# Kernel tuning notes

Hardware: AMD Instinct MI355X
Metric: run time of the kernel (lower is better)

The kernel has to match this reference:

```python
import jax, jax.numpy as jnp
import numpy as np

N = 1048576  # rays * samples per batch
IN_DIM = 32          # hashgrid encoder output (16 levels x 2 feats)
SH_DIM = 16          # degree-4 spherical harmonics
HID = 64
GEO = 15


def sh_encode(v):
    """Real spherical harmonics up to degree 4 (16 comps), v: [N,3] unit vecs."""
    x, y, z = v[..., 0], v[..., 1], v[..., 2]
    xx, yy, zz = x * x, y * y, z * z
    xy, yz, xz = x * y, y * z, x * z
    comps = [
        jnp.full_like(x, 0.28209479177387814),
        -0.48860251190291987 * y,
        0.48860251190291987 * z,
        -0.48860251190291987 * x,
        1.0925484305920792 * xy,
        -1.0925484305920792 * yz,
        0.94617469575755997 * zz - 0.31539156525252005,
        -1.0925484305920792 * xz,
        0.54627421529603959 * (xx - yy),
        0.59004358992664352 * y * (3.0 * xx - yy),
        2.8906114426405538 * xy * z,
        0.45704579946446572 * y * (4.0 * zz - xx - yy),
        0.3731763325901154 * z * (2.0 * zz - 3.0 * xx - 3.0 * yy),
        0.45704579946446572 * x * (4.0 * zz - xx - yy),
        1.445305721320277 * z * (xx - yy),
        0.5900435899266435 * x * (xx - 3.0 * yy),
    ]
    return jnp.stack(comps, axis=-1)


def _w(key, fan_in, fan_out):
    return jax.random.normal(key, (fan_in, fan_out), dtype=jnp.float32) / np.sqrt(fan_in)


def setup_inputs() -> dict:
    key = jax.random.key(0)
    ks = jax.random.split(key, 12)
    x_feat = jax.random.normal(ks[0], (N, IN_DIM), dtype=jnp.float32)
    d = jax.random.normal(ks[1], (N, 3), dtype=jnp.float32)
    d = d / jnp.linalg.norm(d, axis=-1, keepdims=True)
    lig = jax.random.normal(ks[2], (N, 3), dtype=jnp.float32)
    lig = lig / jnp.linalg.norm(lig, axis=-1, keepdims=True)
    return {
        "x_feat": x_feat, "d": d, "lig": lig,
        # sigma net: 32 -> 64 -> 1+15
        "w_sig0": _w(ks[3], IN_DIM, HID),
        "w_sig1": _w(ks[4], HID, 1 + GEO),
        # color net: (16+16+32) -> 64, (64+15) -> 64, 64 -> 3
        "w_col0": _w(ks[5], SH_DIM + SH_DIM + IN_DIM, HID),
        "w_col1": _w(ks[6], HID + GEO, HID),
        "w_col2": _w(ks[7], HID, 3),
        # vis net (only 2 layers run in forward): (16+32) -> 64, 64 -> 1
        "w_vis0": _w(ks[8], SH_DIM + IN_DIM, HID),
        "w_vis1": _w(ks[9], HID, 1),
    }


def reference(x_feat, d, lig, w_sig0, w_sig1, w_col0, w_col1, w_col2, w_vis0, w_vis1):
    # sigma tower (bias-free)
    h = jax.nn.relu(x_feat @ w_sig0)
    h = h @ w_sig1                      # [N, 1+GEO]
    geo_feat = h[..., 1:]               # sigma = trunc_exp(h[...,0]) is unused in output

    d_enc = sh_encode(d)                # [N,16]
    l_enc = sh_encode(lig)              # [N,16]

    # color tower: cat([h_x, light, d]) then cat geo_feat before layer 1
    hc = jnp.concatenate([x_feat, l_enc, d_enc], axis=-1)
    hc = jax.nn.relu(hc @ w_col0)
    hc = jnp.concatenate([hc, geo_feat], axis=-1)
    hc = jax.nn.relu(hc @ w_col1)
    hc = hc @ w_col2
    color = jax.nn.relu(hc)             # [N,3]

    # vis tower: cat([h_x, light]), 2 layers (range(num_layers))
    hv = jnp.concatenate([x_feat, l_enc], axis=-1)
    hv = jax.nn.relu(hv @ w_vis0)
    hv = hv @ w_vis1
    vis = jax.nn.sigmoid(hv)            # [N,1]

    return color * vis                  # broadcast -> [N,3]
```

## Files before the change

kernel.cpp:

```cpp
#include <hip/hip_runtime.h>
#include <math.h>

#define BLOCK 256
#define GRID  512

typedef _Float16 half8 __attribute__((ext_vector_type(8)));
typedef float    f32x4 __attribute__((ext_vector_type(4)));

__device__ __forceinline__ int phi(int nt, int m) {
    return ((nt >> 1) << 5) + ((m >> 2) << 3) + ((nt & 1) << 2) + (m & 3);
}

__device__ __forceinline__ half8 bfragW(const float* __restrict__ w, int N0,
                                        int nsrc, int k0, int Kreal, bool valid) {
    half8 r;
    #pragma unroll
    for (int j = 0; j < 8; j++) {
        int k = k0 + j;
        float v = (valid && k < Kreal) ? w[k * N0 + nsrc] : 0.f;
        r[j] = (_Float16)v;
    }
    return r;
}

__device__ __forceinline__ half8 packrelu(f32x4 a, f32x4 b) {
    half8 h;
    #pragma unroll
    for (int r = 0; r < 4; r++) {
        h[r]     = (_Float16)fmaxf(a[r], 0.f);
        h[4 + r] = (_Float16)fmaxf(b[r], 0.f);
    }
    return h;
}

__device__ __forceinline__ half8 packraw(f32x4 a, f32x4 b) {
    half8 h;
    #pragma unroll
    for (int r = 0; r < 4; r++) {
        h[r]     = (_Float16)a[r];
        h[4 + r] = (_Float16)b[r];
    }
    return h;
}

__device__ __forceinline__ void sh16(float x, float y, float z, float* e) {
    float xx = x * x, yy = y * y, zz = z * z;
    float xy = x * y, yz = y * z, xz = x * z;
    e[0]  = 0.28209479177387814f;
    e[1]  = -0.48860251190291987f * y;
    e[2]  = 0.48860251190291987f * z;
    e[3]  = -0.48860251190291987f * x;
    e[4]  = 1.0925484305920792f * xy;
    e[5]  = -1.0925484305920792f * yz;
    e[6]  = 0.94617469575756f * zz - 0.31539156525252005f;
    e[7]  = -1.0925484305920792f * xz;
    e[8]  = 0.5462742152960396f * (xx - yy);
    e[9]  = 0.5900435899266435f * y * (3.0f * xx - yy);
    e[10] = 2.890611442640554f * xy * z;
    e[11] = 0.4570457994644657f * y * (4.0f * zz - xx - yy);
    e[12] = 0.3731763325901154f * z * (2.0f * zz - 3.0f * xx - 3.0f * yy);
    e[13] = 0.4570457994644657f * x * (4.0f * zz - xx - yy);
    e[14] = 1.445305721320277f * z * (xx - yy);
    e[15] = 0.5900435899266435f * x * (xx - 3.0f * yy);
}

#define MFMA(A, B, C) __builtin_amdgcn_mfma_f32_16x16x32_f16((A), (B), (C), 0, 0, 0)

__global__ __launch_bounds__(BLOCK, 2) void nerf_reg(
    const float* __restrict__ x_feat,
    const float* __restrict__ dvec,
    const float* __restrict__ lvec,
    const float* __restrict__ w_sig0,
    const float* __restrict__ w_sig1,
    const float* __restrict__ w_col0,
    const float* __restrict__ w_col1,
    const float* __restrict__ w_col2,
    const float* __restrict__ w_vis0,
    const float* __restrict__ w_vis1,
    float* __restrict__ out, int n)
{
    const int tid  = threadIdx.x;
    const int wv   = tid >> 6;
    const int lane = tid & 63;
    const int m    = lane & 15;
    const int q    = lane >> 4;

    half8 Wsig0[4], Wcol0[8], Wvis0[8], Wsig1[4], Wvis1[2], Wcol1[12], Wcol2[2];
    #pragma unroll
    for (int nt = 0; nt < 4; nt++)
        Wsig0[nt] = bfragW(w_sig0, 64, phi(nt, m), q * 8, 32, true);
    #pragma unroll
    for (int nt = 0; nt < 4; nt++)
        #pragma unroll
        for (int kt = 0; kt < 2; kt++)
            Wcol0[nt * 2 + kt] = bfragW(w_col0, 64, phi(nt, m), kt * 32 + q * 8, 64, true);
    #pragma unroll
    for (int nt = 0; nt < 4; nt++)
        #pragma unroll
        for (int kt = 0; kt < 2; kt++)
            Wvis0[nt * 2 + kt] = bfragW(w_vis0, 64, phi(nt, m), kt * 32 + q * 8, 48, true);
    #pragma unroll
    for (int nt = 0; nt < 2; nt++)
        #pragma unroll
        for (int kt = 0; kt < 2; kt++) {
            int g = ((m >> 2) << 3) + ((nt & 1) << 2) + (m & 3);
            bool valid = ((m >> 2) < 2) && (g < 15);
            Wsig1[nt * 2 + kt] = bfragW(w_sig1, 16, g + 1, kt * 32 + q * 8, 64, valid);
        }
    #pragma unroll
    for (int kt = 0; kt < 2; kt++)
        Wvis1[kt] = bfragW(w_vis1, 1, 0, kt * 32 + q * 8, 64, m == 0);
    #pragma unroll
    for (int nt = 0; nt < 4; nt++)
        #pragma unroll
        for (int kt = 0; kt < 3; kt++)
            Wcol1[nt * 3 + kt] = bfragW(w_col1, 64, phi(nt, m), kt * 32 + q * 8, 79, true);
    #pragma unroll
    for (int kt = 0; kt < 2; kt++)
        Wcol2[kt] = bfragW(w_col2, 3, m, kt * 32 + q * 8, 64, m < 3);

    const f32x4 z = {0.f, 0.f, 0.f, 0.f};
    const int ntiles = n >> 6;
    for (int t = blockIdx.x; t < ntiles; t += GRID) {
        const int pt = (t << 6) + wv * 16 + m;

        const float4* xv = (const float4*)(x_feat + (size_t)pt * 32 + q * 8);
        float4 v0 = xv[0], v1 = xv[1];
        half8 fI0;
        fI0[0] = (_Float16)v0.x; fI0[1] = (_Float16)v0.y;
        fI0[2] = (_Float16)v0.z; fI0[3] = (_Float16)v0.w;
        fI0[4] = (_Float16)v1.x; fI0[5] = (_Float16)v1.y;
        fI0[6] = (_Float16)v1.z; fI0[7] = (_Float16)v1.w;

        const float* vv = (q < 2 ? lvec : dvec) + (size_t)pt * 3;
        float e[16];
        sh16(vv[0], vv[1], vv[2], e);
        half8 lo, hi;
        #pragma unroll
        for (int u = 0; u < 8; u++) {
            lo[u] = (_Float16)e[u];
            hi[u] = (_Float16)e[8 + u];
        }
        half8 fI1 = (q & 1) ? hi : lo;

        f32x4 a0 = z, a1 = z, a2 = z, a3 = z;
        a0 = MFMA(Wsig0[0], fI0, a0);
        a1 = MFMA(Wsig0[1], fI0, a1);
        a2 = MFMA(Wsig0[2], fI0, a2);
        a3 = MFMA(Wsig0[3], fI0, a3);
        half8 hK0 = packrelu(a0, a1), hK1 = packrelu(a2, a3);

        a0 = z; a1 = z; a2 = z; a3 = z;
        a0 = MFMA(Wcol0[0], fI0, a0); a0 = MFMA(Wcol0[1], fI1, a0);
        a1 = MFMA(Wcol0[2], fI0, a1); a1 = MFMA(Wcol0[3], fI1, a1);
        a2 = MFMA(Wcol0[4], fI0, a2); a2 = MFMA(Wcol0[5], fI1, a2);
        a3 = MFMA(Wcol0[6], fI0, a3); a3 = MFMA(Wcol0[7], fI1, a3);
        half8 cK0 = packrelu(a0, a1), cK1 = packrelu(a2, a3);

        a0 = z; a1 = z; a2 = z; a3 = z;
        a0 = MFMA(Wvis0[0], fI0, a0); a0 = MFMA(Wvis0[1], fI1, a0);
        a1 = MFMA(Wvis0[2], fI0, a1); a1 = MFMA(Wvis0[3], fI1, a1);
        a2 = MFMA(Wvis0[4], fI0, a2); a2 = MFMA(Wvis0[5], fI1, a2);
        a3 = MFMA(Wvis0[6], fI0, a3); a3 = MFMA(Wvis0[7], fI1, a3);
        half8 vK0 = packrelu(a0, a1), vK1 = packrelu(a2, a3);

        a0 = z; a1 = z;
        a0 = MFMA(Wsig1[0], hK0, a0); a0 = MFMA(Wsig1[1], hK1, a0);
        a1 = MFMA(Wsig1[2], hK0, a1); a1 = MFMA(Wsig1[3], hK1, a1);
        half8 gK2 = packraw(a0, a1);

        f32x4 av = z;
        av = MFMA(Wvis1[0], vK0, av);
        av = MFMA(Wvis1[1], vK1, av);
        float vis = 1.f / (1.f + expf(-av[0]));

        a0 = z; a1 = z; a2 = z; a3 = z;
        a0 = MFMA(Wcol1[0], cK0, a0); a0 = MFMA(Wcol1[1], cK1, a0); a0 = MFMA(Wcol1[2], gK2, a0);
        a1 = MFMA(Wcol1[3], cK0, a1); a1 = MFMA(Wcol1[4], cK1, a1); a1 = MFMA(Wcol1[5], gK2, a1);
        a2 = MFMA(Wcol1[6], cK0, a2); a2 = MFMA(Wcol1[7], cK1, a2); a2 = MFMA(Wcol1[8], gK2, a2);
        a3 = MFMA(Wcol1[9], cK0, a3); a3 = MFMA(Wcol1[10], cK1, a3); a3 = MFMA(Wcol1[11], gK2, a3);
        half8 h2K0 = packrelu(a0, a1), h2K1 = packrelu(a2, a3);

        f32x4 ac = z;
        ac = MFMA(Wcol2[0], h2K0, ac);
        ac = MFMA(Wcol2[1], h2K1, ac);
        if (q == 0) {
            float* o = out + (size_t)pt * 3;
            o[0] = fmaxf(ac[0], 0.f) * vis;
            o[1] = fmaxf(ac[1], 0.f) * vis;
            o[2] = fmaxf(ac[2], 0.f) * vis;
        }
    }
}

extern "C" void kernel_launch(void* const* d_in, const int* in_sizes, int n_in,
                              void* d_out, int out_size, void* d_ws, size_t ws_size,
                              hipStream_t stream) {
    const float* x_feat = (const float*)d_in[0];
    const float* dvec   = (const float*)d_in[1];
    const float* lvec   = (const float*)d_in[2];
    const float* w_sig0 = (const float*)d_in[3];
    const float* w_sig1 = (const float*)d_in[4];
    const float* w_col0 = (const float*)d_in[5];
    const float* w_col1 = (const float*)d_in[6];
    const float* w_col2 = (const float*)d_in[7];
    const float* w_vis0 = (const float*)d_in[8];
    const float* w_vis1 = (const float*)d_in[9];
    float* out = (float*)d_out;

    const int n = in_sizes[0] / 32;
    nerf_reg<<<GRID, BLOCK, 0, stream>>>(x_feat, dvec, lvec,
                                         w_sig0, w_sig1, w_col0, w_col1,
                                         w_col2, w_vis0, w_vis1, out, n);
}
```

Baseline: 291.5 us.

## Stage MLP weight fragments in LDS and process two 16-point tiles per wave

Weight fragments move from per-thread registers into shared memory, loaded once per block by the four waves in parallel and read back per MFMA. Each wave now handles two 16-point tiles per iteration, so every LDS weight read feeds two MFMAs. Launch bounds rise to 3 blocks per CU and the grid grows to 2048 blocks. The aim is lower register pressure and higher occupancy to hide global load latency, at the cost of LDS traffic inside the inner loop and more live activation registers for the second tile.

```diff
diff --git a/kernel.cpp b/kernel.cpp
--- a/kernel.cpp
+++ b/kernel.cpp
@@ -2,7 +2,7 @@
 #include <math.h>
 
 #define BLOCK 256
-#define GRID  512
+#define GRID  2048
 
 typedef _Float16 half8 __attribute__((ext_vector_type(8)));
 typedef float    f32x4 __attribute__((ext_vector_type(4)));
@@ -66,7 +66,16 @@
 
 #define MFMA(A, B, C) __builtin_amdgcn_mfma_f32_16x16x32_f16((A), (B), (C), 0, 0, 0)
 
-__global__ __launch_bounds__(BLOCK, 2) void nerf_reg(
+#define NFRAG  40
+#define F_SIG0 0
+#define F_COL0 4
+#define F_VIS0 12
+#define F_SIG1 20
+#define F_VIS1 24
+#define F_COL1 26
+#define F_COL2 38
+
+__global__ __launch_bounds__(BLOCK, 3) void nerf_lds(
     const float* __restrict__ x_feat,
     const float* __restrict__ dvec,
     const float* __restrict__ lvec,
@@ -85,112 +94,180 @@
     const int m    = lane & 15;
     const int q    = lane >> 4;
 
-    half8 Wsig0[4], Wcol0[8], Wvis0[8], Wsig1[4], Wvis1[2], Wcol1[12], Wcol2[2];
-    #pragma unroll
-    for (int nt = 0; nt < 4; nt++)
-        Wsig0[nt] = bfragW(w_sig0, 64, phi(nt, m), q * 8, 32, true);
-    #pragma unroll
-    for (int nt = 0; nt < 4; nt++)
+    __shared__ half8 WL[NFRAG * 64];
+
+    if (wv == 0) {
+        #pragma unroll
+        for (int nt = 0; nt < 4; nt++)
+            WL[(F_SIG0 + nt) * 64 + lane] =
+                bfragW(w_sig0, 64, phi(nt, m), q * 8, 32, true);
+        #pragma unroll
+        for (int nt = 0; nt < 2; nt++)
+            #pragma unroll
+            for (int kt = 0; kt < 2; kt++) {
+                int g = ((m >> 2) << 3) + ((nt & 1) << 2) + (m & 3);
+                bool valid = ((m >> 2) < 2) && (g < 15);
+                WL[(F_SIG1 + nt * 2 + kt) * 64 + lane] =
+                    bfragW(w_sig1, 16, g + 1, kt * 32 + q * 8, 64, valid);
+            }
         #pragma unroll
         for (int kt = 0; kt < 2; kt++)
-            Wcol0[nt * 2 + kt] = bfragW(w_col0, 64, phi(nt, m), kt * 32 + q * 8, 64, true);
-    #pragma unroll
-    for (int nt = 0; nt < 4; nt++)
+            WL[(F_VIS1 + kt) * 64 + lane] =
+                bfragW(w_vis1, 1, 0, kt * 32 + q * 8, 64, m == 0);
+    } else if (wv == 1) {
+        #pragma unroll
+        for (int nt = 0; nt < 4; nt++)
+            #pragma unroll
+            for (int kt = 0; kt < 2; kt++)
+                WL[(F_COL0 + nt * 2 + kt) * 64 + lane] =
+                    bfragW(w_col0, 64, phi(nt, m), kt * 32 + q * 8, 64, true);
         #pragma unroll
         for (int kt = 0; kt < 2; kt++)
-            Wvis0[nt * 2 + kt] = bfragW(w_vis0, 64, phi(nt, m), kt * 32 + q * 8, 48, true);
-    #pragma unroll
-    for (int nt = 0; nt < 2; nt++)
-        #pragma unroll
-        for (int kt = 0; kt < 2; kt++) {
-            int g = ((m >> 2) << 3) + ((nt & 1) << 2) + (m & 3);
-            bool valid = ((m >> 2) < 2) && (g < 15);
-            Wsig1[nt * 2 + kt] = bfragW(w_sig1, 16, g + 1, kt * 32 + q * 8, 64, valid);
+            WL[(F_COL2 + kt) * 64 + lane] =
+                bfragW(w_col2, 3, m, kt * 32 + q * 8, 64, m < 3);
+    } else if (wv == 2) {
+        #pragma unroll
+        for (int nt = 0; nt < 4; nt++)
+            #pragma unroll
+            for (int kt = 0; kt < 2; kt++)
+                WL[(F_VIS0 + nt * 2 + kt) * 64 + lane] =
+                    bfragW(w_vis0, 64, phi(nt, m), kt * 32 + q * 8, 48, true);
+    } else {
+        #pragma unroll
+        for (int nt = 0; nt < 4; nt++)
+            #pragma unroll
+            for (int kt = 0; kt < 3; kt++)
+                WL[(F_COL1 + nt * 3 + kt) * 64 + lane] =
+                    bfragW(w_col1, 64, phi(nt, m), kt * 32 + q * 8, 79, true);
+    }
+    __syncthreads();
+
+    int wl = lane;
+    #define LW(f) WL[wl + (f) * 64]
+
+    const f32x4 z = {0.f, 0.f, 0.f, 0.f};
+    const int ntiles = n >> 7;
+    for (int t = blockIdx.x; t < ntiles; t += GRID) {
+        asm volatile("" : "+v"(wl));
+
+        const int pt0 = (t << 7) + wv * 32 + m;
+        const int pt1 = pt0 + 16;
+
+        half8 fA0, fB0;
+        {
+            const float4* xa = (const float4*)(x_feat + (size_t)pt0 * 32 + q * 8);
+            float4 v0 = xa[0], v1 = xa[1];
+            fA0[0] = (_Float16)v0.x; fA0[1] = (_Float16)v0.y;
+            fA0[2] = (_Float16)v0.z; fA0[3] = (_Float16)v0.w;
+            fA0[4] = (_Float16)v1.x; fA0[5] = (_Float16)v1.y;
+            fA0[6] = (_Float16)v1.z; fA0[7] = (_Float16)v1.w;
+            const float4* xb = (const float4*)(x_feat + (size_t)pt1 * 32 + q * 8);
+            float4 u0 = xb[0], u1 = xb[1];
+            fB0[0] = (_Float16)u0.x; fB0[1] = (_Float16)u0.y;
+            fB0[2] = (_Float16)u0.z; fB0[3] = (_Float16)u0.w;
+            fB0[4] = (_Float16)u1.x; fB0[5] = (_Float16)u1.y;
+            fB0[6] = (_Float16)u1.z; fB0[7] = (_Float16)u1.w;
         }
-    #pragma unroll
-    for (int kt = 0; kt < 2; kt++)
-        Wvis1[kt] = bfragW(w_vis1, 1, 0, kt * 32 + q * 8, 64, m == 0);
-    #pragma unroll
-    for (int nt = 0; nt < 4; nt++)
-        #pragma unroll
-        for (int kt = 0; kt < 3; kt++)
-            Wcol1[nt * 3 + kt] = bfragW(w_col1, 64, phi(nt, m), kt * 32 + q * 8, 79, true);
-    #pragma unroll
-    for (int kt = 0; kt < 2; kt++)
-        Wcol2[kt] = bfragW(w_col2, 3, m, kt * 32 + q * 8, 64, m < 3);
-
-    const f32x4 z = {0.f, 0.f, 0.f, 0.f};
-    const int ntiles = n >> 6;
-    for (int t = blockIdx.x; t < ntiles; t += GRID) {
-        const int pt = (t << 6) + wv * 16 + m;
-
-        const float4* xv = (const float4*)(x_feat + (size_t)pt * 32 + q * 8);
-        float4 v0 = xv[0], v1 = xv[1];
-        half8 fI0;
-        fI0[0] = (_Float16)v0.x; fI0[1] = (_Float16)v0.y;
-        fI0[2] = (_Float16)v0.z; fI0[3] = (_Float16)v0.w;
-        fI0[4] = (_Float16)v1.x; fI0[5] = (_Float16)v1.y;
-        fI0[6] = (_Float16)v1.z; fI0[7] = (_Float16)v1.w;
-
-        const float* vv = (q < 2 ? lvec : dvec) + (size_t)pt * 3;
-        float e[16];
-        sh16(vv[0], vv[1], vv[2], e);
-        half8 lo, hi;
-        #pragma unroll
-        for (int u = 0; u < 8; u++) {
-            lo[u] = (_Float16)e[u];
-            hi[u] = (_Float16)e[8 + u];
+
+        half8 fA1, fB1;
+        {
+            const float* va = (q < 2 ? lvec : dvec) + (size_t)pt0 * 3;
+            float ea[16];
+            sh16(va[0], va[1], va[2], ea);
+            #pragma unroll
+            for (int u = 0; u < 8; u++) {
+                float s = (q & 1) ? ea[8 + u] : ea[u];
+                fA1[u] = (_Float16)s;
+            }
+            const float* vb = (q < 2 ? lvec : dvec) + (size_t)pt1 * 3;
+            float eb[16];
+            sh16(vb[0], vb[1], vb[2], eb);
+            #pragma unroll
+            for (int u = 0; u < 8; u++) {
+                float s = (q & 1) ? eb[8 + u] : eb[u];
+                fB1[u] = (_Float16)s;
+            }
         }
-        half8 fI1 = (q & 1) ? hi : lo;
-
-        f32x4 a0 = z, a1 = z, a2 = z, a3 = z;
-        a0 = MFMA(Wsig0[0], fI0, a0);
-        a1 = MFMA(Wsig0[1], fI0, a1);
-        a2 = MFMA(Wsig0[2], fI0, a2);
-        a3 = MFMA(Wsig0[3], fI0, a3);
-        half8 hK0 = packrelu(a0, a1), hK1 = packrelu(a2, a3);
-
-        a0 = z; a1 = z; a2 = z; a3 = z;
-        a0 = MFMA(Wcol0[0], fI0, a0); a0 = MFMA(Wcol0[1], fI1, a0);
-        a1 = MFMA(Wcol0[2], fI0, a1); a1 = MFMA(Wcol0[3], fI1, a1);
-        a2 = MFMA(Wcol0[4], fI0, a2); a2 = MFMA(Wcol0[5], fI1, a2);
-        a3 = MFMA(Wcol0[6], fI0, a3); a3 = MFMA(Wcol0[7], fI1, a3);
-        half8 cK0 = packrelu(a0, a1), cK1 = packrelu(a2, a3);
-
-        a0 = z; a1 = z; a2 = z; a3 = z;
-        a0 = MFMA(Wvis0[0], fI0, a0); a0 = MFMA(Wvis0[1], fI1, a0);
-        a1 = MFMA(Wvis0[2], fI0, a1); a1 = MFMA(Wvis0[3], fI1, a1);
-        a2 = MFMA(Wvis0[4], fI0, a2); a2 = MFMA(Wvis0[5], fI1, a2);
-        a3 = MFMA(Wvis0[6], fI0, a3); a3 = MFMA(Wvis0[7], fI1, a3);
-        half8 vK0 = packrelu(a0, a1), vK1 = packrelu(a2, a3);
-
-        a0 = z; a1 = z;
-        a0 = MFMA(Wsig1[0], hK0, a0); a0 = MFMA(Wsig1[1], hK1, a0);
-        a1 = MFMA(Wsig1[2], hK0, a1); a1 = MFMA(Wsig1[3], hK1, a1);
-        half8 gK2 = packraw(a0, a1);
-
-        f32x4 av = z;
-        av = MFMA(Wvis1[0], vK0, av);
-        av = MFMA(Wvis1[1], vK1, av);
-        float vis = 1.f / (1.f + expf(-av[0]));
-
-        a0 = z; a1 = z; a2 = z; a3 = z;
-        a0 = MFMA(Wcol1[0], cK0, a0); a0 = MFMA(Wcol1[1], cK1, a0); a0 = MFMA(Wcol1[2], gK2, a0);
-        a1 = MFMA(Wcol1[3], cK0, a1); a1 = MFMA(Wcol1[4], cK1, a1); a1 = MFMA(Wcol1[5], gK2, a1);
-        a2 = MFMA(Wcol1[6], cK0, a2); a2 = MFMA(Wcol1[7], cK1, a2); a2 = MFMA(Wcol1[8], gK2, a2);
-        a3 = MFMA(Wcol1[9], cK0, a3); a3 = MFMA(Wcol1[10], cK1, a3); a3 = MFMA(Wcol1[11], gK2, a3);
-        half8 h2K0 = packrelu(a0, a1), h2K1 = packrelu(a2, a3);
-
-        f32x4 ac = z;
-        ac = MFMA(Wcol2[0], h2K0, ac);
-        ac = MFMA(Wcol2[1], h2K1, ac);
+
+        f32x4 a0, a1, a2, a3, b0, b1, b2, b3;
+        half8 w;
+
+        a0 = z; a1 = z; a2 = z; a3 = z; b0 = z; b1 = z; b2 = z; b3 = z;
+        w = LW(F_SIG0 + 0); a0 = MFMA(w, fA0, a0); b0 = MFMA(w, fB0, b0);
+        w = LW(F_SIG0 + 1); a1 = MFMA(w, fA0, a1); b1 = MFMA(w, fB0, b1);
+        w = LW(F_SIG0 + 2); a2 = MFMA(w, fA0, a2); b2 = MFMA(w, fB0, b2);
+        w = LW(F_SIG0 + 3); a3 = MFMA(w, fA0, a3); b3 = MFMA(w, fB0, b3);
+        half8 hK0a = packrelu(a0, a1), hK1a = packrelu(a2, a3);
+        half8 hK0b = packrelu(b0, b1), hK1b = packrelu(b2, b3);
+
+        a0 = z; a1 = z; a2 = z; a3 = z; b0 = z; b1 = z; b2 = z; b3 = z;
+        w = LW(F_COL0 + 0); a0 = MFMA(w, fA0, a0); b0 = MFMA(w, fB0, b0);
+        w = LW(F_COL0 + 1); a0 = MFMA(w, fA1, a0); b0 = MFMA(w, fB1, b0);
+        w = LW(F_COL0 + 2); a1 = MFMA(w, fA0, a1); b1 = MFMA(w, fB0, b1);
+        w = LW(F_COL0 + 3); a1 = MFMA(w, fA1, a1); b1 = MFMA(w, fB1, b1);
+        w = LW(F_COL0 + 4); a2 = MFMA(w, fA0, a2); b2 = MFMA(w, fB0, b2);
+        w = LW(F_COL0 + 5); a2 = MFMA(w, fA1, a2); b2 = MFMA(w, fB1, b2);
+        w = LW(F_COL0 + 6); a3 = MFMA(w, fA0, a3); b3 = MFMA(w, fB0, b3);
+        w = LW(F_COL0 + 7); a3 = MFMA(w, fA1, a3); b3 = MFMA(w, fB1, b3);
+        half8 cK0a = packrelu(a0, a1), cK1a = packrelu(a2, a3);
+        half8 cK0b = packrelu(b0, b1), cK1b = packrelu(b2, b3);
+
+        a0 = z; a1 = z; a2 = z; a3 = z; b0 = z; b1 = z; b2 = z; b3 = z;
+        w = LW(F_VIS0 + 0); a0 = MFMA(w, fA0, a0); b0 = MFMA(w, fB0, b0);
+        w = LW(F_VIS0 + 1); a0 = MFMA(w, fA1, a0); b0 = MFMA(w, fB1, b0);
+        w = LW(F_VIS0 + 2); a1 = MFMA(w, fA0, a1); b1 = MFMA(w, fB0, b1);
+        w = LW(F_VIS0 + 3); a1 = MFMA(w, fA1, a1); b1 = MFMA(w, fB1, b1);
+        w = LW(F_VIS0 + 4); a2 = MFMA(w, fA0, a2); b2 = MFMA(w, fB0, b2);
+        w = LW(F_VIS0 + 5); a2 = MFMA(w, fA1, a2); b2 = MFMA(w, fB1, b2);
+        w = LW(F_VIS0 + 6); a3 = MFMA(w, fA0, a3); b3 = MFMA(w, fB0, b3);
+        w = LW(F_VIS0 + 7); a3 = MFMA(w, fA1, a3); b3 = MFMA(w, fB1, b3);
+        half8 vK0a = packrelu(a0, a1), vK1a = packrelu(a2, a3);
+        half8 vK0b = packrelu(b0, b1), vK1b = packrelu(b2, b3);
+
+        a0 = z; a1 = z; b0 = z; b1 = z;
+        w = LW(F_SIG1 + 0); a0 = MFMA(w, hK0a, a0); b0 = MFMA(w, hK0b, b0);
+        w = LW(F_SIG1 + 1); a0 = MFMA(w, hK1a, a0); b0 = MFMA(w, hK1b, b0);
+        w = LW(F_SIG1 + 2); a1 = MFMA(w, hK0a, a1); b1 = MFMA(w, hK0b, b1);
+        w = LW(F_SIG1 + 3); a1 = MFMA(w, hK1a, a1); b1 = MFMA(w, hK1b, b1);
+        half8 gA = packraw(a0, a1), gB = packraw(b0, b1);
+
+        f32x4 va = z, vb = z;
+        w = LW(F_VIS1 + 0); va = MFMA(w, vK0a, va); vb = MFMA(w, vK0b, vb);
+        w = LW(F_VIS1 + 1); va = MFMA(w, vK1a, va); vb = MFMA(w, vK1b, vb);
+        float visA = 1.f / (1.f + expf(-va[0]));
+        float visB = 1.f / (1.f + expf(-vb[0]));
+
+        a0 = z; a1 = z; a2 = z; a3 = z; b0 = z; b1 = z; b2 = z; b3 = z;
+        w = LW(F_COL1 + 0);  a0 = MFMA(w, cK0a, a0); b0 = MFMA(w, cK0b, b0);
+        w = LW(F_COL1 + 1);  a0 = MFMA(w, cK1a, a0); b0 = MFMA(w, cK1b, b0);
+        w = LW(F_COL1 + 2);  a0 = MFMA(w, gA,   a0); b0 = MFMA(w, gB,   b0);
+        w = LW(F_COL1 + 3);  a1 = MFMA(w, cK0a, a1); b1 = MFMA(w, cK0b, b1);
+        w = LW(F_COL1 + 4);  a1 = MFMA(w, cK1a, a1); b1 = MFMA(w, cK1b, b1);
+        w = LW(F_COL1 + 5);  a1 = MFMA(w, gA,   a1); b1 = MFMA(w, gB,   b1);
+        w = LW(F_COL1 + 6);  a2 = MFMA(w, cK0a, a2); b2 = MFMA(w, cK0b, b2);
+        w = LW(F_COL1 + 7);  a2 = MFMA(w, cK1a, a2); b2 = MFMA(w, cK1b, b2);
+        w = LW(F_COL1 + 8);  a2 = MFMA(w, gA,   a2); b2 = MFMA(w, gB,   b2);
+        w = LW(F_COL1 + 9);  a3 = MFMA(w, cK0a, a3); b3 = MFMA(w, cK0b, b3);
+        w = LW(F_COL1 + 10); a3 = MFMA(w, cK1a, a3); b3 = MFMA(w, cK1b, b3);
+        w = LW(F_COL1 + 11); a3 = MFMA(w, gA,   a3); b3 = MFMA(w, gB,   b3);
+        half8 h2K0a = packrelu(a0, a1), h2K1a = packrelu(a2, a3);
+        half8 h2K0b = packrelu(b0, b1), h2K1b = packrelu(b2, b3);
+
+        f32x4 ca = z, cb = z;
+        w = LW(F_COL2 + 0); ca = MFMA(w, h2K0a, ca); cb = MFMA(w, h2K0b, cb);
+        w = LW(F_COL2 + 1); ca = MFMA(w, h2K1a, ca); cb = MFMA(w, h2K1b, cb);
         if (q == 0) {
-            float* o = out + (size_t)pt * 3;
-            o[0] = fmaxf(ac[0], 0.f) * vis;
-            o[1] = fmaxf(ac[1], 0.f) * vis;
-            o[2] = fmaxf(ac[2], 0.f) * vis;
+            float* oa = out + (size_t)pt0 * 3;
+            oa[0] = fmaxf(ca[0], 0.f) * visA;
+            oa[1] = fmaxf(ca[1], 0.f) * visA;
+            oa[2] = fmaxf(ca[2], 0.f) * visA;
+            float* ob = out + (size_t)pt1 * 3;
+            ob[0] = fmaxf(cb[0], 0.f) * visB;
+            ob[1] = fmaxf(cb[1], 0.f) * visB;
+            ob[2] = fmaxf(cb[2], 0.f) * visB;
         }
     }
+    #undef LW
 }
 
 extern "C" void kernel_launch(void* const* d_in, const int* in_sizes, int n_in,
@@ -209,7 +286,7 @@
     float* out = (float*)d_out;
 
     const int n = in_sizes[0] / 32;
-    nerf_reg<<<GRID, BLOCK, 0, stream>>>(x_feat, dvec, lvec,
+    nerf_lds<<<GRID, BLOCK, 0, stream>>>(x_feat, dvec, lvec,
                                          w_sig0, w_sig1, w_col0, w_col1,
                                          w_col2, w_vis0, w_vis1, out, n);
 }
```

After: 277.0 us. 1.05x faster.

## Stage weight fragments in LDS instead of registers to raise occupancy

Applied to the files above, without the earlier changes.

Moves the 40 per-lane MFMA weight fragments out of VGPRs into a shared-memory table built cooperatively by the four waves, then reloads each fragment from LDS right before its MFMA. This frees a large block of registers so launch bounds can request four blocks per CU, and the grid grows from 512 to 4096 blocks to fill them. The sigma second layer is also reordered earlier. In exchange, every tile now issues about 40 LDS reads and each block rebuilds the weight table from global memory.

```diff
diff --git a/kernel.cpp b/kernel.cpp
--- a/kernel.cpp
+++ b/kernel.cpp
@@ -2,7 +2,7 @@
 #include <math.h>
 
 #define BLOCK 256
-#define GRID  512
+#define GRID  4096
 
 typedef _Float16 half8 __attribute__((ext_vector_type(8)));
 typedef float    f32x4 __attribute__((ext_vector_type(4)));
@@ -66,7 +66,16 @@
 
 #define MFMA(A, B, C) __builtin_amdgcn_mfma_f32_16x16x32_f16((A), (B), (C), 0, 0, 0)
 
-__global__ __launch_bounds__(BLOCK, 2) void nerf_reg(
+#define NFRAG  40
+#define F_SIG0 0
+#define F_COL0 4
+#define F_VIS0 12
+#define F_SIG1 20
+#define F_VIS1 24
+#define F_COL1 26
+#define F_COL2 38
+
+__global__ __launch_bounds__(BLOCK, 4) void nerf_lds1(
     const float* __restrict__ x_feat,
     const float* __restrict__ dvec,
     const float* __restrict__ lvec,
@@ -85,43 +94,62 @@
     const int m    = lane & 15;
     const int q    = lane >> 4;
 
-    half8 Wsig0[4], Wcol0[8], Wvis0[8], Wsig1[4], Wvis1[2], Wcol1[12], Wcol2[2];
-    #pragma unroll
-    for (int nt = 0; nt < 4; nt++)
-        Wsig0[nt] = bfragW(w_sig0, 64, phi(nt, m), q * 8, 32, true);
-    #pragma unroll
-    for (int nt = 0; nt < 4; nt++)
+    __shared__ half8 WL[NFRAG * 64];
+
+    if (wv == 0) {
+        #pragma unroll
+        for (int nt = 0; nt < 4; nt++)
+            WL[(F_SIG0 + nt) * 64 + lane] =
+                bfragW(w_sig0, 64, phi(nt, m), q * 8, 32, true);
+        #pragma unroll
+        for (int nt = 0; nt < 2; nt++)
+            #pragma unroll
+            for (int kt = 0; kt < 2; kt++) {
+                int g = ((m >> 2) << 3) + ((nt & 1) << 2) + (m & 3);
+                bool valid = ((m >> 2) < 2) && (g < 15);
+                WL[(F_SIG1 + nt * 2 + kt) * 64 + lane] =
+                    bfragW(w_sig1, 16, g + 1, kt * 32 + q * 8, 64, valid);
+            }
         #pragma unroll
         for (int kt = 0; kt < 2; kt++)
-            Wcol0[nt * 2 + kt] = bfragW(w_col0, 64, phi(nt, m), kt * 32 + q * 8, 64, true);
-    #pragma unroll
-    for (int nt = 0; nt < 4; nt++)
+            WL[(F_VIS1 + kt) * 64 + lane] =
+                bfragW(w_vis1, 1, 0, kt * 32 + q * 8, 64, m == 0);
+    } else if (wv == 1) {
+        #pragma unroll
+        for (int nt = 0; nt < 4; nt++)
+            #pragma unroll
+            for (int kt = 0; kt < 2; kt++)
+                WL[(F_COL0 + nt * 2 + kt) * 64 + lane] =
+                    bfragW(w_col0, 64, phi(nt, m), kt * 32 + q * 8, 64, true);
         #pragma unroll
         for (int kt = 0; kt < 2; kt++)
-            Wvis0[nt * 2 + kt] = bfragW(w_vis0, 64, phi(nt, m), kt * 32 + q * 8, 48, true);
-    #pragma unroll
-    for (int nt = 0; nt < 2; nt++)
-        #pragma unroll
-        for (int kt = 0; kt < 2; kt++) {
-            int g = ((m >> 2) << 3) + ((nt & 1) << 2) + (m & 3);
-            bool valid = ((m >> 2) < 2) && (g < 15);
-            Wsig1[nt * 2 + kt] = bfragW(w_sig1, 16, g + 1, kt * 32 + q * 8, 64, valid);
-        }
-    #pragma unroll
-    for (int kt = 0; kt < 2; kt++)
-        Wvis1[kt] = bfragW(w_vis1, 1, 0, kt * 32 + q * 8, 64, m == 0);
-    #pragma unroll
-    for (int nt = 0; nt < 4; nt++)
-        #pragma unroll
-        for (int kt = 0; kt < 3; kt++)
-            Wcol1[nt * 3 + kt] = bfragW(w_col1, 64, phi(nt, m), kt * 32 + q * 8, 79, true);
-    #pragma unroll
-    for (int kt = 0; kt < 2; kt++)
-        Wcol2[kt] = bfragW(w_col2, 3, m, kt * 32 + q * 8, 64, m < 3);
+            WL[(F_COL2 + kt) * 64 + lane] =
+                bfragW(w_col2, 3, m, kt * 32 + q * 8, 64, m < 3);
+    } else if (wv == 2) {
+        #pragma unroll
+        for (int nt = 0; nt < 4; nt++)
+            #pragma unroll
+            for (int kt = 0; kt < 2; kt++)
+                WL[(F_VIS0 + nt * 2 + kt) * 64 + lane] =
+                    bfragW(w_vis0, 64, phi(nt, m), kt * 32 + q * 8, 48, true);
+    } else {
+        #pragma unroll
+        for (int nt = 0; nt < 4; nt++)
+            #pragma unroll
+            for (int kt = 0; kt < 3; kt++)
+                WL[(F_COL1 + nt * 3 + kt) * 64 + lane] =
+                    bfragW(w_col1, 64, phi(nt, m), kt * 32 + q * 8, 79, true);
+    }
+    __syncthreads();
+
+    int wl = lane;
+    #define LW(f) WL[wl + (f) * 64]
 
     const f32x4 z = {0.f, 0.f, 0.f, 0.f};
     const int ntiles = n >> 6;
     for (int t = blockIdx.x; t < ntiles; t += GRID) {
+        asm volatile("" : "+v"(wl));
+
         const int pt = (t << 6) + wv * 16 + m;
 
         const float4* xv = (const float4*)(x_feat + (size_t)pt * 32 + q * 8);
@@ -135,55 +163,75 @@
         const float* vv = (q < 2 ? lvec : dvec) + (size_t)pt * 3;
         float e[16];
         sh16(vv[0], vv[1], vv[2], e);
-        half8 lo, hi;
+        half8 fI1;
         #pragma unroll
         for (int u = 0; u < 8; u++) {
-            lo[u] = (_Float16)e[u];
-            hi[u] = (_Float16)e[8 + u];
+            float s = (q & 1) ? e[8 + u] : e[u];
+            fI1[u] = (_Float16)s;
         }
-        half8 fI1 = (q & 1) ? hi : lo;
-
-        f32x4 a0 = z, a1 = z, a2 = z, a3 = z;
-        a0 = MFMA(Wsig0[0], fI0, a0);
-        a1 = MFMA(Wsig0[1], fI0, a1);
-        a2 = MFMA(Wsig0[2], fI0, a2);
-        a3 = MFMA(Wsig0[3], fI0, a3);
+
+        f32x4 a0, a1, a2, a3;
+        half8 w;
+
+        a0 = z; a1 = z; a2 = z; a3 = z;
+        w = LW(F_SIG0 + 0); a0 = MFMA(w, fI0, a0);
+        w = LW(F_SIG0 + 1); a1 = MFMA(w, fI0, a1);
+        w = LW(F_SIG0 + 2); a2 = MFMA(w, fI0, a2);
+        w = LW(F_SIG0 + 3); a3 = MFMA(w, fI0, a3);
         half8 hK0 = packrelu(a0, a1), hK1 = packrelu(a2, a3);
 
-        a0 = z; a1 = z; a2 = z; a3 = z;
-        a0 = MFMA(Wcol0[0], fI0, a0); a0 = MFMA(Wcol0[1], fI1, a0);
-        a1 = MFMA(Wcol0[2], fI0, a1); a1 = MFMA(Wcol0[3], fI1, a1);
-        a2 = MFMA(Wcol0[4], fI0, a2); a2 = MFMA(Wcol0[5], fI1, a2);
-        a3 = MFMA(Wcol0[6], fI0, a3); a3 = MFMA(Wcol0[7], fI1, a3);
+        a0 = z; a1 = z;
+        w = LW(F_SIG1 + 0); a0 = MFMA(w, hK0, a0);
+        w = LW(F_SIG1 + 1); a0 = MFMA(w, hK1, a0);
+        w = LW(F_SIG1 + 2); a1 = MFMA(w, hK0, a1);
+        w = LW(F_SIG1 + 3); a1 = MFMA(w, hK1, a1);
+        half8 gK2 = packraw(a0, a1);
+
+        a0 = z; a1 = z; a2 = z; a3 = z;
+        w = LW(F_COL0 + 0); a0 = MFMA(w, fI0, a0);
+        w = LW(F_COL0 + 1); a0 = MFMA(w, fI1, a0);
+        w = LW(F_COL0 + 2); a1 = MFMA(w, fI0, a1);
+        w = LW(F_COL0 + 3); a1 = MFMA(w, fI1, a1);
+        w = LW(F_COL0 + 4); a2 = MFMA(w, fI0, a2);
+        w = LW(F_COL0 + 5); a2 = MFMA(w, fI1, a2);
+        w = LW(F_COL0 + 6); a3 = MFMA(w, fI0, a3);
+        w = LW(F_COL0 + 7); a3 = MFMA(w, fI1, a3);
         half8 cK0 = packrelu(a0, a1), cK1 = packrelu(a2, a3);
 
         a0 = z; a1 = z; a2 = z; a3 = z;
-        a0 = MFMA(Wvis0[0], fI0, a0); a0 = MFMA(Wvis0[1], fI1, a0);
-        a1 = MFMA(Wvis0[2], fI0, a1); a1 = MFMA(Wvis0[3], fI1, a1);
-        a2 = MFMA(Wvis0[4], fI0, a2); a2 = MFMA(Wvis0[5], fI1, a2);
-        a3 = MFMA(Wvis0[6], fI0, a3); a3 = MFMA(Wvis0[7], fI1, a3);
+        w = LW(F_VIS0 + 0); a0 = MFMA(w, fI0, a0);
+        w = LW(F_VIS0 + 1); a0 = MFMA(w, fI1, a0);
+        w = LW(F_VIS0 + 2); a1 = MFMA(w, fI0, a1);
+        w = LW(F_VIS0 + 3); a1 = MFMA(w, fI1, a1);
+        w = LW(F_VIS0 + 4); a2 = MFMA(w, fI0, a2);
+        w = LW(F_VIS0 + 5); a2 = MFMA(w, fI1, a2);
+        w = LW(F_VIS0 + 6); a3 = MFMA(w, fI0, a3);
+        w = LW(F_VIS0 + 7); a3 = MFMA(w, fI1, a3);
         half8 vK0 = packrelu(a0, a1), vK1 = packrelu(a2, a3);
 
-        a0 = z; a1 = z;
-        a0 = MFMA(Wsig1[0], hK0, a0); a0 = MFMA(Wsig1[1], hK1, a0);
-        a1 = MFMA(Wsig1[2], hK0, a1); a1 = MFMA(Wsig1[3], hK1, a1);
-        half8 gK2 = packraw(a0, a1);
-
         f32x4 av = z;
-        av = MFMA(Wvis1[0], vK0, av);
-        av = MFMA(Wvis1[1], vK1, av);
+        w = LW(F_VIS1 + 0); av = MFMA(w, vK0, av);
+        w = LW(F_VIS1 + 1); av = MFMA(w, vK1, av);
         float vis = 1.f / (1.f + expf(-av[0]));
 
         a0 = z; a1 = z; a2 = z; a3 = z;
-        a0 = MFMA(Wcol1[0], cK0, a0); a0 = MFMA(Wcol1[1], cK1, a0); a0 = MFMA(Wcol1[2], gK2, a0);
-        a1 = MFMA(Wcol1[3], cK0, a1); a1 = MFMA(Wcol1[4], cK1, a1); a1 = MFMA(Wcol1[5], gK2, a1);
-        a2 = MFMA(Wcol1[6], cK0, a2); a2 = MFMA(Wcol1[7], cK1, a2); a2 = MFMA(Wcol1[8], gK2, a2);
-        a3 = MFMA(Wcol1[9], cK0, a3); a3 = MFMA(Wcol1[10], cK1, a3); a3 = MFMA(Wcol1[11], gK2, a3);
+        w = LW(F_COL1 + 0);  a0 = MFMA(w, cK0, a0);
+        w = LW(F_COL1 + 1);  a0 = MFMA(w, cK1, a0);
+        w = LW(F_COL1 + 2);  a0 = MFMA(w, gK2, a0);
+        w = LW(F_COL1 + 3);  a1 = MFMA(w, cK0, a1);
+        w = LW(F_COL1 + 4);  a1 = MFMA(w, cK1, a1);
+        w = LW(F_COL1 + 5);  a1 = MFMA(w, gK2, a1);
+        w = LW(F_COL1 + 6);  a2 = MFMA(w, cK0, a2);
+        w = LW(F_COL1 + 7);  a2 = MFMA(w, cK1, a2);
+        w = LW(F_COL1 + 8);  a2 = MFMA(w, gK2, a2);
+        w = LW(F_COL1 + 9);  a3 = MFMA(w, cK0, a3);
+        w = LW(F_COL1 + 10); a3 = MFMA(w, cK1, a3);
+        w = LW(F_COL1 + 11); a3 = MFMA(w, gK2, a3);
         half8 h2K0 = packrelu(a0, a1), h2K1 = packrelu(a2, a3);
 
         f32x4 ac = z;
-        ac = MFMA(Wcol2[0], h2K0, ac);
-        ac = MFMA(Wcol2[1], h2K1, ac);
+        w = LW(F_COL2 + 0); ac = MFMA(w, h2K0, ac);
+        w = LW(F_COL2 + 1); ac = MFMA(w, h2K1, ac);
         if (q == 0) {
             float* o = out + (size_t)pt * 3;
             o[0] = fmaxf(ac[0], 0.f) * vis;
@@ -191,6 +239,7 @@
             o[2] = fmaxf(ac[2], 0.f) * vis;
         }
     }
+    #undef LW
 }
 
 extern "C" void kernel_launch(void* const* d_in, const int* in_sizes, int n_in,
@@ -209,7 +258,7 @@
     float* out = (float*)d_out;
 
     const int n = in_sizes[0] / 32;
-    nerf_reg<<<GRID, BLOCK, 0, stream>>>(x_feat, dvec, lvec,
-                                         w_sig0, w_sig1, w_col0, w_col1,
-                                         w_col2, w_vis0, w_vis1, out, n);
-}
+    nerf_lds1<<<GRID, BLOCK, 0, stream>>>(x_feat, dvec, lvec,
+                                          w_sig0, w_sig1, w_col0, w_col1,
+                                          w_col2, w_vis0, w_vis1, out, n);
+}
```

Measured after the change: 289.8 us. Within noise of the previous version (-0.6%).
